# Optimization experiments

Hardware: AMD Instinct MI355X
Metric: run time of the kernel (lower is better)

Reference implementation:

```python
import jax, jax.numpy as jnp
import numpy as np

GROUP_SIZE = 128  # in_features // scales.shape[1]


def setup_inputs() -> dict:
    key = jax.random.key(0)
    kA, kq, ks, kz, kb = jax.random.split(key, 5)
    M, K, N = 2048, 4096, 4096
    G = K // GROUP_SIZE  # 32 groups
    A = jax.random.normal(kA, (M, K), dtype=jnp.float32)
    # unpacked uint4 quantized weights, values in [0, 16)
    qweight = jax.random.randint(kq, (N, K), 0, 16, dtype=jnp.int32)
    # per-group scales (typical GPTQ magnitude) and zero-points (float, 'original' zeros_mode)
    scales = jax.random.uniform(ks, (N, G), dtype=jnp.float32) * 0.02
    zeros = jax.random.uniform(kz, (N, G), dtype=jnp.float32) * 15.0
    bias = jax.random.normal(kb, (N,), dtype=jnp.float32)
    return {"A": A, "qweight": qweight, "scales": scales, "zeros": zeros, "bias": bias}


def reference(A, qweight, scales, zeros, bias):
    # Dequant: W[n,k] = (q[n,k] - zeros[n, k//gs]) * scales[n, k//gs]
    N, K = qweight.shape
    gs = K // scales.shape[1]
    s = jnp.repeat(scales, gs, axis=1)  # [N, K]
    z = jnp.repeat(zeros, gs, axis=1)   # [N, K]
    W = (qweight.astype(A.dtype) - z) * s
    # out[m,n] = sum_k A[m,k] * W[n,k] + bias[n]
    return jnp.einsum("mk,nk->mn", A, W) + bias
```

## Files before the change

kernel.cpp:

```cpp
#include <hip/hip_runtime.h>
#include <cstdint>
#include <cstddef>

#define MM 2048
#define KK 4096
#define NN 4096
#define GG 32
#define BM 128
#define BN 256
#define BK 64
#define NTILES (KK / BK)

typedef _Float16 half8_t __attribute__((ext_vector_type(8)));
typedef _Float16 half4_t __attribute__((ext_vector_type(4)));
typedef float f32x4 __attribute__((ext_vector_type(4)));

__device__ __forceinline__ void load_lds16(const void* gptr, void* lptr) {
  __builtin_amdgcn_global_load_lds(
      (const __attribute__((address_space(1))) unsigned int*)gptr,
      (__attribute__((address_space(3))) unsigned int*)lptr, 16, 0, 0);
}

#define ACNT8 (MM * KK / 8)
__global__ void prep_kernel(const float* __restrict__ A, const int* __restrict__ q,
                            const float* __restrict__ scales, const float* __restrict__ zeros,
                            _Float16* __restrict__ Ah, _Float16* __restrict__ Wh) {
  const int i = blockIdx.x * blockDim.x + threadIdx.x;
  if (i < ACNT8) {
    const float4 v0 = ((const float4*)A)[2 * (size_t)i];
    const float4 v1 = ((const float4*)A)[2 * (size_t)i + 1];
    half8_t h;
    h[0] = (_Float16)v0.x; h[1] = (_Float16)v0.y; h[2] = (_Float16)v0.z; h[3] = (_Float16)v0.w;
    h[4] = (_Float16)v1.x; h[5] = (_Float16)v1.y; h[6] = (_Float16)v1.z; h[7] = (_Float16)v1.w;
    *(half8_t*)(Ah + 8 * (size_t)i) = h;
  } else {
    const int j = i - ACNT8;
    const int e = j << 3;
    const int n = e >> 12;
    const int k = e & (KK - 1);
    const int g = k >> 7;
    const float sc = scales[(n << 5) + g];
    const float zp = zeros[(n << 5) + g];
    const float nzs = -zp * sc;
    const int4 q0 = ((const int4*)q)[2 * (size_t)j];
    const int4 q1 = ((const int4*)q)[2 * (size_t)j + 1];
    half8_t h;
    h[0] = (_Float16)fmaf((float)q0.x, sc, nzs);
    h[1] = (_Float16)fmaf((float)q0.y, sc, nzs);
    h[2] = (_Float16)fmaf((float)q0.z, sc, nzs);
    h[3] = (_Float16)fmaf((float)q0.w, sc, nzs);
    h[4] = (_Float16)fmaf((float)q1.x, sc, nzs);
    h[5] = (_Float16)fmaf((float)q1.y, sc, nzs);
    h[6] = (_Float16)fmaf((float)q1.z, sc, nzs);
    h[7] = (_Float16)fmaf((float)q1.w, sc, nzs);
    *(half8_t*)(Wh + (size_t)e) = h;
  }
}

__global__ __launch_bounds__(512, 2)
void gemm8_kernel(const _Float16* __restrict__ Ah, const _Float16* __restrict__ Wh,
                  const float* __restrict__ bias, float* __restrict__ out)
{
  __shared__ __align__(16) _Float16 sA[3][BM * BK];
  __shared__ __align__(16) _Float16 sB[3][BN * BK];

  const int tid = threadIdx.x;
  const int lane = tid & 63;
  const int wave = tid >> 6;
  const int wr = wave >> 2;
  const int wc = wave & 3;
  const int lr = lane & 15, quad = lane >> 4;

  const int bid = blockIdx.x;
  const int xcd = bid & 7;
  const int slot = bid >> 3;
  const int mt = slot >> 1;
  const int nt = xcd * 2 + (slot & 1);
  const int m0 = mt * BM;
  const int n0 = nt * BN;

  const int srow = lane >> 3, scc = lane & 7, gch = scc ^ srow;

  f32x4 acc[4][4];
#pragma unroll
  for (int i = 0; i < 4; ++i)
#pragma unroll
    for (int j = 0; j < 4; ++j) acc[i][j] = (f32x4){0.f, 0.f, 0.f, 0.f};

  auto stageA = [&](int t, int buf, int i) {
    load_lds16(Ah + (size_t)(m0 + i * 64 + (wave << 3) + srow) * KK + t * BK + (gch << 3),
               (void*)&sA[buf][(i * 64 + (wave << 3)) * BK]);
  };
  auto stageB = [&](int t, int buf, int i) {
    load_lds16(Wh + (size_t)(n0 + i * 64 + (wave << 3) + srow) * KK + t * BK + (gch << 3),
               (void*)&sB[buf][(i * 64 + (wave << 3)) * BK]);
  };

  stageB(0, 0, 0); stageB(0, 0, 1); stageA(0, 0, 0);
  stageB(0, 0, 2); stageB(0, 0, 3); stageA(0, 0, 1);
  stageB(1, 1, 0); stageB(1, 1, 1); stageA(1, 1, 0);
  stageB(1, 1, 2); stageB(1, 1, 3); stageA(1, 1, 1);
  asm volatile("s_waitcnt vmcnt(6)" ::: "memory");
  __builtin_amdgcn_s_barrier();

  int cur = 0, nb = 2;
  for (int t = 0; t < NTILES; ++t) {
    const _Float16* pA = sA[cur];
    const _Float16* pB = sB[cur];
    const bool st = (t < NTILES - 2);
    half8_t a0[2][2], a1[2][2], b[4][2];

#pragma unroll
    for (int x = 0; x < 2; ++x) {
      const _Float16* ba = &pA[(wr * 64 + x * 16 + lr) * BK];
#pragma unroll
      for (int ks = 0; ks < 2; ++ks)
        a0[x][ks] = *(const half8_t*)&ba[((ks * 4 + quad) ^ (lr & 7)) * 8];
    }
#pragma unroll
    for (int ni = 0; ni < 4; ++ni) {
      const _Float16* bb = &pB[(wc * 64 + ni * 16 + lr) * BK];
#pragma unroll
      for (int ks = 0; ks < 2; ++ks)
        b[ni][ks] = *(const half8_t*)&bb[((ks * 4 + quad) ^ (lr & 7)) * 8];
    }
    if (st) { stageB(t + 2, nb, 0); stageB(t + 2, nb, 1); stageA(t + 2, nb, 0); }
    __builtin_amdgcn_sched_barrier(0);
    __builtin_amdgcn_s_barrier();
    __builtin_amdgcn_s_setprio(1);
#pragma unroll
    for (int x = 0; x < 2; ++x)
#pragma unroll
      for (int ni = 0; ni < 4; ++ni) {
        acc[x][ni] = __builtin_amdgcn_mfma_f32_16x16x32_f16(a0[x][0], b[ni][0], acc[x][ni], 0, 0, 0);
        acc[x][ni] = __builtin_amdgcn_mfma_f32_16x16x32_f16(a0[x][1], b[ni][1], acc[x][ni], 0, 0, 0);
      }
    __builtin_amdgcn_s_setprio(0);
    __builtin_amdgcn_s_barrier();

#pragma unroll
    for (int x = 0; x < 2; ++x) {
      const _Float16* ba = &pA[(wr * 64 + (x + 2) * 16 + lr) * BK];
#pragma unroll
      for (int ks = 0; ks < 2; ++ks)
        a1[x][ks] = *(const half8_t*)&ba[((ks * 4 + quad) ^ (lr & 7)) * 8];
    }
    if (st) { stageB(t + 2, nb, 2); stageB(t + 2, nb, 3); stageA(t + 2, nb, 1); }
    __builtin_amdgcn_sched_barrier(0);
    __builtin_amdgcn_s_barrier();
    __builtin_amdgcn_s_setprio(1);
#pragma unroll
    for (int x = 0; x < 2; ++x)
#pragma unroll
      for (int ni = 0; ni < 4; ++ni) {
        acc[x + 2][ni] = __builtin_amdgcn_mfma_f32_16x16x32_f16(a1[x][0], b[ni][0], acc[x + 2][ni], 0, 0, 0);
        acc[x + 2][ni] = __builtin_amdgcn_mfma_f32_16x16x32_f16(a1[x][1], b[ni][1], acc[x + 2][ni], 0, 0, 0);
      }
    __builtin_amdgcn_s_setprio(0);
    if (t < NTILES - 2) asm volatile("s_waitcnt vmcnt(6)" ::: "memory");
    else                asm volatile("s_waitcnt vmcnt(0)" ::: "memory");
    __builtin_amdgcn_s_barrier();
    cur = (cur == 2) ? 0 : cur + 1;
    nb  = (nb  == 2) ? 0 : nb + 1;
  }

#pragma unroll
  for (int ni = 0; ni < 4; ++ni) {
    const int n = n0 + wc * 64 + ni * 16 + lr;
    const float bv = bias[n];
#pragma unroll
    for (int mi = 0; mi < 4; ++mi) {
      const int mbase = m0 + wr * 64 + mi * 16 + quad * 4;
#pragma unroll
      for (int r = 0; r < 4; ++r)
        out[(size_t)(mbase + r) * NN + n] = acc[mi][ni][r] + bv;
    }
  }
}

__global__ __launch_bounds__(256, 2)
void gemm_fused_kernel(const float* __restrict__ Af, const int* __restrict__ qw,
                       const float* __restrict__ scales, const float* __restrict__ zeros,
                       const float* __restrict__ bias, float* __restrict__ out)
{
  __shared__ __align__(16) _Float16 sA[128 * 64];
  __shared__ __align__(16) _Float16 sB[128 * 64];

  const int tid = threadIdx.x;
  const int lane = tid & 63;
  const int wave = tid >> 6;
  const int wr = wave >> 1, wc = wave & 1;

  const int bid = blockIdx.x;
  const int xcd = bid & 7;
  const int slot = bid >> 3;
  const int mt = slot >> 2;
  const int nt = xcd * 4 + (slot & 3);
  const int m0 = mt * 128;
  const int n0 = nt * 128;

  const int lr = lane & 15, quad = lane >> 4;

  f32x4 acc[4][4];
#pragma unroll
  for (int i = 0; i < 4; ++i)
#pragma unroll
    for (int j = 0; j < 4; ++j) acc[i][j] = (f32x4){0.f, 0.f, 0.f, 0.f};

  const int frow = tid >> 4;
  const int fc4 = tid & 15;

  for (int kt = 0; kt < KK / 64; ++kt) {
    const int k0 = kt * 64;
    const int g = k0 >> 7;
#pragma unroll
    for (int p = 0; p < 8; ++p) {
      const int row = p * 16 + frow;
      const int pc = (fc4 >> 1) ^ (row & 7);
      const int dst = row * 64 + pc * 8 + (fc4 & 1) * 4;
      const float4 avf = *(const float4*)&Af[(size_t)(m0 + row) * KK + k0 + fc4 * 4];
      half4_t ah;
      ah[0] = (_Float16)avf.x; ah[1] = (_Float16)avf.y;
      ah[2] = (_Float16)avf.z; ah[3] = (_Float16)avf.w;
      *(half4_t*)&sA[dst] = ah;
      const int n = n0 + row;
      const float sc = scales[(n << 5) + g];
      const float zp = zeros[(n << 5) + g];
      const float nzs = -zp * sc;
      const int4 qv = *(const int4*)&qw[(size_t)n * KK + k0 + fc4 * 4];
      half4_t bh;
      bh[0] = (_Float16)fmaf((float)qv.x, sc, nzs);
      bh[1] = (_Float16)fmaf((float)qv.y, sc, nzs);
      bh[2] = (_Float16)fmaf((float)qv.z, sc, nzs);
      bh[3] = (_Float16)fmaf((float)qv.w, sc, nzs);
      *(half4_t*)&sB[dst] = bh;
    }
    __syncthreads();
#pragma unroll
    for (int ks = 0; ks < 2; ++ks) {
      half8_t a[4], b[4];
#pragma unroll
      for (int t = 0; t < 4; ++t) {
        const int rA = wr * 64 + t * 16 + lr;
        const int j = ks * 4 + quad;
        a[t] = *(const half8_t*)&sA[rA * 64 + ((j ^ (lr & 7)) * 8)];
        const int rB = wc * 64 + t * 16 + lr;
        b[t] = *(const half8_t*)&sB[rB * 64 + ((j ^ (lr & 7)) * 8)];
      }
#pragma unroll
      for (int mi = 0; mi < 4; ++mi)
#pragma unroll
        for (int ni = 0; ni < 4; ++ni)
          acc[mi][ni] = __builtin_amdgcn_mfma_f32_16x16x32_f16(a[mi], b[ni], acc[mi][ni], 0, 0, 0);
    }
    __syncthreads();
  }

#pragma unroll
  for (int ni = 0; ni < 4; ++ni) {
    const int n = n0 + wc * 64 + ni * 16 + lr;
    const float bv = bias[n];
#pragma unroll
    for (int mi = 0; mi < 4; ++mi) {
      const int mbase = m0 + wr * 64 + mi * 16 + quad * 4;
#pragma unroll
      for (int r = 0; r < 4; ++r)
        out[(size_t)(mbase + r) * NN + n] = acc[mi][ni][r] + bv;
    }
  }
}

extern "C" void kernel_launch(void* const* d_in, const int* in_sizes, int n_in,
                              void* d_out, int out_size, void* d_ws, size_t ws_size,
                              hipStream_t stream) {
  (void)in_sizes; (void)n_in; (void)out_size;
  const float* A      = (const float*)d_in[0];
  const int*   qw     = (const int*)d_in[1];
  const float* scales = (const float*)d_in[2];
  const float* zeros  = (const float*)d_in[3];
  const float* bias   = (const float*)d_in[4];
  float* out = (float*)d_out;

  const size_t needA = (size_t)MM * KK * sizeof(_Float16);
  const size_t needW = (size_t)NN * KK * sizeof(_Float16);

  if (ws_size >= needA + needW) {
    _Float16* Ah = (_Float16*)d_ws;
    _Float16* Wh = (_Float16*)((char*)d_ws + needA);
    prep_kernel<<<((MM + NN) * KK / 8) / 256, 256, 0, stream>>>(A, qw, scales, zeros, Ah, Wh);
    gemm8_kernel<<<dim3(MM / BM * NN / BN), dim3(512), 0, stream>>>(Ah, Wh, bias, out);
  } else {
    gemm_fused_kernel<<<dim3(512), dim3(256), 0, stream>>>(A, qw, scales, zeros, bias, out);
  }
}
```

Before: 207.7 us.

## Store weights as uint8 and dequantize in-register inside the GEMM mainloop

The prep kernel now packs the int32 quantized weights to bytes and writes a transposed table of fp16 scale/offset pairs, instead of materializing a full fp16 weight matrix. The GEMM stages the byte weights and all scale/offset pairs into LDS, then dequantizes each fragment in registers using the 0x6400 magic-number fp16 trick before the MFMAs. This halves the weight traffic written by prep and read by the GEMM. In exchange it adds ALU work to the inner loop, rebalances the staging schedule and wait counts, and moves scale and offset math to fp16, which changes rounding.

```diff
diff --git a/kernel.cpp b/kernel.cpp
--- a/kernel.cpp
+++ b/kernel.cpp
@@ -13,6 +13,7 @@
 
 typedef _Float16 half8_t __attribute__((ext_vector_type(8)));
 typedef _Float16 half4_t __attribute__((ext_vector_type(4)));
+typedef _Float16 half2_t __attribute__((ext_vector_type(2)));
 typedef float f32x4 __attribute__((ext_vector_type(4)));
 
 __device__ __forceinline__ void load_lds16(const void* gptr, void* lptr) {
@@ -21,10 +22,35 @@
       (__attribute__((address_space(3))) unsigned int*)lptr, 16, 0, 0);
 }
 
+__device__ __forceinline__ half2_t h2_from_u32(unsigned v) {
+  union { unsigned u; half2_t h; } x; x.u = v; return x.h;
+}
+
+__device__ __forceinline__ half8_t dq8(unsigned d0, unsigned d1,
+                                       half2_t s2, half2_t c2) {
+  const unsigned M = 0x64006400u;
+  const half2_t off = (half2_t){(_Float16)1024.0f, (_Float16)1024.0f};
+  unsigned u0 = M | ((d0 & 0xFFu)         | ((d0 & 0xFF00u) << 8));
+  unsigned u1 = M | (((d0 >> 16) & 0xFFu) | ((d0 >> 24) << 16));
+  unsigned u2 = M | ((d1 & 0xFFu)         | ((d1 & 0xFF00u) << 8));
+  unsigned u3 = M | (((d1 >> 16) & 0xFFu) | ((d1 >> 24) << 16));
+  half2_t w0 = (h2_from_u32(u0) - off) * s2 + c2;
+  half2_t w1 = (h2_from_u32(u1) - off) * s2 + c2;
+  half2_t w2 = (h2_from_u32(u2) - off) * s2 + c2;
+  half2_t w3 = (h2_from_u32(u3) - off) * s2 + c2;
+  half8_t r;
+  r[0] = w0[0]; r[1] = w0[1]; r[2] = w1[0]; r[3] = w1[1];
+  r[4] = w2[0]; r[5] = w2[1]; r[6] = w3[0]; r[7] = w3[1];
+  return r;
+}
+
 #define ACNT8 (MM * KK / 8)
+#define WCNT8 (NN * KK / 8)
+#define SZCNT (NN * GG)
 __global__ void prep_kernel(const float* __restrict__ A, const int* __restrict__ q,
                             const float* __restrict__ scales, const float* __restrict__ zeros,
-                            _Float16* __restrict__ Ah, _Float16* __restrict__ Wh) {
+                            _Float16* __restrict__ Ah, unsigned char* __restrict__ Wq,
+                            unsigned* __restrict__ SZT) {
   const int i = blockIdx.x * blockDim.x + threadIdx.x;
   if (i < ACNT8) {
     const float4 v0 = ((const float4*)A)[2 * (size_t)i];
@@ -33,36 +59,35 @@
     h[0] = (_Float16)v0.x; h[1] = (_Float16)v0.y; h[2] = (_Float16)v0.z; h[3] = (_Float16)v0.w;
     h[4] = (_Float16)v1.x; h[5] = (_Float16)v1.y; h[6] = (_Float16)v1.z; h[7] = (_Float16)v1.w;
     *(half8_t*)(Ah + 8 * (size_t)i) = h;
-  } else {
+  } else if (i < ACNT8 + WCNT8) {
     const int j = i - ACNT8;
-    const int e = j << 3;
-    const int n = e >> 12;
-    const int k = e & (KK - 1);
-    const int g = k >> 7;
-    const float sc = scales[(n << 5) + g];
-    const float zp = zeros[(n << 5) + g];
-    const float nzs = -zp * sc;
     const int4 q0 = ((const int4*)q)[2 * (size_t)j];
     const int4 q1 = ((const int4*)q)[2 * (size_t)j + 1];
-    half8_t h;
-    h[0] = (_Float16)fmaf((float)q0.x, sc, nzs);
-    h[1] = (_Float16)fmaf((float)q0.y, sc, nzs);
-    h[2] = (_Float16)fmaf((float)q0.z, sc, nzs);
-    h[3] = (_Float16)fmaf((float)q0.w, sc, nzs);
-    h[4] = (_Float16)fmaf((float)q1.x, sc, nzs);
-    h[5] = (_Float16)fmaf((float)q1.y, sc, nzs);
-    h[6] = (_Float16)fmaf((float)q1.z, sc, nzs);
-    h[7] = (_Float16)fmaf((float)q1.w, sc, nzs);
-    *(half8_t*)(Wh + (size_t)e) = h;
+    uint2 p;
+    p.x = (q0.x & 0xFFu) | ((q0.y & 0xFFu) << 8) | ((q0.z & 0xFFu) << 16) | ((unsigned)(q0.w & 0xFFu) << 24);
+    p.y = (q1.x & 0xFFu) | ((q1.y & 0xFFu) << 8) | ((q1.z & 0xFFu) << 16) | ((unsigned)(q1.w & 0xFFu) << 24);
+    ((uint2*)Wq)[j] = p;
+  } else {
+    const int e = i - ACNT8 - WCNT8;
+    const int n = e >> 5;
+    const int g = e & 31;
+    const float s = scales[e];
+    const float z = zeros[e];
+    const float c = -z * s;
+    union { _Float16 h; unsigned short u; } sh, ch;
+    sh.h = (_Float16)s; ch.h = (_Float16)c;
+    SZT[(size_t)g * NN + n] = (unsigned)sh.u | ((unsigned)ch.u << 16);
   }
 }
 
 __global__ __launch_bounds__(512, 2)
-void gemm8_kernel(const _Float16* __restrict__ Ah, const _Float16* __restrict__ Wh,
+void gemm8_kernel(const _Float16* __restrict__ Ah, const unsigned char* __restrict__ Wq,
+                  const unsigned* __restrict__ SZT,
                   const float* __restrict__ bias, float* __restrict__ out)
 {
   __shared__ __align__(16) _Float16 sA[3][BM * BK];
-  __shared__ __align__(16) _Float16 sB[3][BN * BK];
+  __shared__ __align__(16) unsigned char sBq[3][BN * BK];
+  __shared__ __align__(16) unsigned sSZ[GG * BN];
 
   const int tid = threadIdx.x;
   const int lane = tid & 63;
@@ -79,7 +104,8 @@
   const int m0 = mt * BM;
   const int n0 = nt * BN;
 
-  const int srow = lane >> 3, scc = lane & 7, gch = scc ^ srow;
+  const int srow = lane >> 3, scc = lane & 7, gchA = scc ^ srow;
+  const int brow = lane >> 2, bcc = lane & 3;
 
   f32x4 acc[4][4];
 #pragma unroll
@@ -88,26 +114,40 @@
     for (int j = 0; j < 4; ++j) acc[i][j] = (f32x4){0.f, 0.f, 0.f, 0.f};
 
   auto stageA = [&](int t, int buf, int i) {
-    load_lds16(Ah + (size_t)(m0 + i * 64 + (wave << 3) + srow) * KK + t * BK + (gch << 3),
+    load_lds16(Ah + (size_t)(m0 + i * 64 + (wave << 3) + srow) * KK + t * BK + (gchA << 3),
                (void*)&sA[buf][(i * 64 + (wave << 3)) * BK]);
   };
-  auto stageB = [&](int t, int buf, int i) {
-    load_lds16(Wh + (size_t)(n0 + i * 64 + (wave << 3) + srow) * KK + t * BK + (gch << 3),
-               (void*)&sB[buf][(i * 64 + (wave << 3)) * BK]);
+  auto stageB = [&](int t, int buf, int c) {
+    const int r = c * 128 + (wave << 4) + brow;
+    const int g16 = bcc ^ ((r >> 1) & 3);
+    load_lds16(Wq + (size_t)(n0 + r) * KK + t * BK + g16 * 16,
+               (void*)&sBq[buf][(c * 128 + (wave << 4)) * BK]);
   };
-
-  stageB(0, 0, 0); stageB(0, 0, 1); stageA(0, 0, 0);
-  stageB(0, 0, 2); stageB(0, 0, 3); stageA(0, 0, 1);
-  stageB(1, 1, 0); stageB(1, 1, 1); stageA(1, 1, 0);
-  stageB(1, 1, 2); stageB(1, 1, 3); stageA(1, 1, 1);
-  asm volatile("s_waitcnt vmcnt(6)" ::: "memory");
+  auto stageSZ = [&](int c) {
+    const int g = c * 8 + wave;
+    load_lds16(SZT + (size_t)g * NN + n0 + lane * 4, (void*)&sSZ[g * BN]);
+  };
+
+  stageSZ(0); stageSZ(1); stageSZ(2); stageSZ(3);
+  stageB(0, 0, 0); stageB(0, 0, 1); stageA(0, 0, 0); stageA(0, 0, 1);
+  stageB(1, 1, 0); stageB(1, 1, 1); stageA(1, 1, 0); stageA(1, 1, 1);
+  asm volatile("s_waitcnt vmcnt(4)" ::: "memory");
   __builtin_amdgcn_s_barrier();
 
+  unsigned szv[4];
   int cur = 0, nb = 2;
   for (int t = 0; t < NTILES; ++t) {
     const _Float16* pA = sA[cur];
-    const _Float16* pB = sB[cur];
+    const unsigned char* pB = sBq[cur];
     const bool st = (t < NTILES - 2);
+
+    if ((t & 1) == 0) {
+      const int g = t >> 1;
+#pragma unroll
+      for (int ni = 0; ni < 4; ++ni)
+        szv[ni] = sSZ[g * BN + wc * 64 + ni * 16 + lr];
+    }
+
     half8_t a0[2][2], a1[2][2], b[4][2];
 
 #pragma unroll
@@ -119,12 +159,18 @@
     }
 #pragma unroll
     for (int ni = 0; ni < 4; ++ni) {
-      const _Float16* bb = &pB[(wc * 64 + ni * 16 + lr) * BK];
-#pragma unroll
-      for (int ks = 0; ks < 2; ++ks)
-        b[ni][ks] = *(const half8_t*)&bb[((ks * 4 + quad) ^ (lr & 7)) * 8];
-    }
-    if (st) { stageB(t + 2, nb, 0); stageB(t + 2, nb, 1); stageA(t + 2, nb, 0); }
+      const int row = wc * 64 + ni * 16 + lr;
+      const half2_t sc = h2_from_u32(szv[ni]);
+      const half2_t s2 = (half2_t){sc[0], sc[0]};
+      const half2_t c2 = (half2_t){sc[1], sc[1]};
+#pragma unroll
+      for (int ks = 0; ks < 2; ++ks) {
+        const int p8 = (ks * 4 + quad) ^ (row & 6);
+        const uint2 d = *(const uint2*)&pB[row * BK + p8 * 8];
+        b[ni][ks] = dq8(d.x, d.y, s2, c2);
+      }
+    }
+    if (st) { stageB(t + 2, nb, 0); stageB(t + 2, nb, 1); }
     __builtin_amdgcn_sched_barrier(0);
     __builtin_amdgcn_s_barrier();
     __builtin_amdgcn_s_setprio(1);
@@ -145,7 +191,7 @@
       for (int ks = 0; ks < 2; ++ks)
         a1[x][ks] = *(const half8_t*)&ba[((ks * 4 + quad) ^ (lr & 7)) * 8];
     }
-    if (st) { stageB(t + 2, nb, 2); stageB(t + 2, nb, 3); stageA(t + 2, nb, 1); }
+    if (st) { stageA(t + 2, nb, 0); stageA(t + 2, nb, 1); }
     __builtin_amdgcn_sched_barrier(0);
     __builtin_amdgcn_s_barrier();
     __builtin_amdgcn_s_setprio(1);
@@ -157,7 +203,7 @@
         acc[x + 2][ni] = __builtin_amdgcn_mfma_f32_16x16x32_f16(a1[x][1], b[ni][1], acc[x + 2][ni], 0, 0, 0);
       }
     __builtin_amdgcn_s_setprio(0);
-    if (t < NTILES - 2) asm volatile("s_waitcnt vmcnt(6)" ::: "memory");
+    if (t < NTILES - 2) asm volatile("s_waitcnt vmcnt(4)" ::: "memory");
     else                asm volatile("s_waitcnt vmcnt(0)" ::: "memory");
     __builtin_amdgcn_s_barrier();
     cur = (cur == 2) ? 0 : cur + 1;
@@ -281,14 +327,16 @@
   const float* bias   = (const float*)d_in[4];
   float* out = (float*)d_out;
 
-  const size_t needA = (size_t)MM * KK * sizeof(_Float16);
-  const size_t needW = (size_t)NN * KK * sizeof(_Float16);
-
-  if (ws_size >= needA + needW) {
-    _Float16* Ah = (_Float16*)d_ws;
-    _Float16* Wh = (_Float16*)((char*)d_ws + needA);
-    prep_kernel<<<((MM + NN) * KK / 8) / 256, 256, 0, stream>>>(A, qw, scales, zeros, Ah, Wh);
-    gemm8_kernel<<<dim3(MM / BM * NN / BN), dim3(512), 0, stream>>>(Ah, Wh, bias, out);
+  const size_t needA  = (size_t)MM * KK * sizeof(_Float16);
+  const size_t needWq = (size_t)NN * KK;
+  const size_t needSZ = (size_t)NN * GG * sizeof(unsigned);
+
+  if (ws_size >= needA + needWq + needSZ) {
+    _Float16*      Ah  = (_Float16*)d_ws;
+    unsigned char* Wq  = (unsigned char*)d_ws + needA;
+    unsigned*      SZT = (unsigned*)((char*)d_ws + needA + needWq);
+    prep_kernel<<<(ACNT8 + WCNT8 + SZCNT) / 256, 256, 0, stream>>>(A, qw, scales, zeros, Ah, Wq, SZT);
+    gemm8_kernel<<<dim3(MM / BM * NN / BN), dim3(512), 0, stream>>>(Ah, Wq, SZT, bias, out);
   } else {
     gemm_fused_kernel<<<dim3(512), dim3(256), 0, stream>>>(A, qw, scales, zeros, bias, out);
   }
```

Result: slower. 239.1 us (+15.1%).

## Use 4-wave blocks with 64x128 warp tiles and BK=32 single-phase loop

Applied to the files above, without the earlier changes.

Rewrites the fp16 GEMM main kernel to use 256 threads (4 waves), each computing a 64x128 output tile with 32 accumulators, and halves the K tile to 32. Each iteration now issues one MFMA phase with a single barrier instead of two split phases with several barriers. The swizzled LDS layout is dropped in favour of plain row addressing. The aim is more MFMA work per LDS fragment load and fewer barriers per tile. The costs are higher register pressure, twice as many K iterations, and possible LDS bank conflicts from the unswizzled reads.

```diff
diff --git a/kernel.cpp b/kernel.cpp
--- a/kernel.cpp
+++ b/kernel.cpp
@@ -8,7 +8,7 @@
 #define GG 32
 #define BM 128
 #define BN 256
-#define BK 64
+#define BK 32
 #define NTILES (KK / BK)
 
 typedef _Float16 half8_t __attribute__((ext_vector_type(8)));
@@ -57,9 +57,9 @@
   }
 }
 
-__global__ __launch_bounds__(512, 2)
-void gemm8_kernel(const _Float16* __restrict__ Ah, const _Float16* __restrict__ Wh,
-                  const float* __restrict__ bias, float* __restrict__ out)
+__global__ __launch_bounds__(256, 2)
+void gemm12_kernel(const _Float16* __restrict__ Ah, const _Float16* __restrict__ Wh,
+                   const float* __restrict__ bias, float* __restrict__ out)
 {
   __shared__ __align__(16) _Float16 sA[3][BM * BK];
   __shared__ __align__(16) _Float16 sB[3][BN * BK];
@@ -67,8 +67,8 @@
   const int tid = threadIdx.x;
   const int lane = tid & 63;
   const int wave = tid >> 6;
-  const int wr = wave >> 2;
-  const int wc = wave & 3;
+  const int wr = wave >> 1;
+  const int wc = wave & 1;
   const int lr = lane & 15, quad = lane >> 4;
 
   const int bid = blockIdx.x;
@@ -79,27 +79,29 @@
   const int m0 = mt * BM;
   const int n0 = nt * BN;
 
-  const int srow = lane >> 3, scc = lane & 7, gch = scc ^ srow;
-
-  f32x4 acc[4][4];
+  const int srow = lane >> 2, sch = lane & 3;
+
+  f32x4 acc[4][8];
 #pragma unroll
   for (int i = 0; i < 4; ++i)
 #pragma unroll
-    for (int j = 0; j < 4; ++j) acc[i][j] = (f32x4){0.f, 0.f, 0.f, 0.f};
+    for (int j = 0; j < 8; ++j) acc[i][j] = (f32x4){0.f, 0.f, 0.f, 0.f};
 
   auto stageA = [&](int t, int buf, int i) {
-    load_lds16(Ah + (size_t)(m0 + i * 64 + (wave << 3) + srow) * KK + t * BK + (gch << 3),
-               (void*)&sA[buf][(i * 64 + (wave << 3)) * BK]);
+    const int r16 = (wave * 2 + i) * 16;
+    load_lds16(Ah + (size_t)(m0 + r16 + srow) * KK + t * BK + sch * 8,
+               (void*)&sA[buf][r16 * BK]);
   };
-  auto stageB = [&](int t, int buf, int i) {
-    load_lds16(Wh + (size_t)(n0 + i * 64 + (wave << 3) + srow) * KK + t * BK + (gch << 3),
-               (void*)&sB[buf][(i * 64 + (wave << 3)) * BK]);
+  auto stageB = [&](int t, int buf, int c) {
+    const int r16 = (wave * 4 + c) * 16;
+    load_lds16(Wh + (size_t)(n0 + r16 + srow) * KK + t * BK + sch * 8,
+               (void*)&sB[buf][r16 * BK]);
   };
 
-  stageB(0, 0, 0); stageB(0, 0, 1); stageA(0, 0, 0);
-  stageB(0, 0, 2); stageB(0, 0, 3); stageA(0, 0, 1);
-  stageB(1, 1, 0); stageB(1, 1, 1); stageA(1, 1, 0);
-  stageB(1, 1, 2); stageB(1, 1, 3); stageA(1, 1, 1);
+  stageB(0, 0, 0); stageB(0, 0, 1); stageB(0, 0, 2); stageB(0, 0, 3);
+  stageA(0, 0, 0); stageA(0, 0, 1);
+  stageB(1, 1, 0); stageB(1, 1, 1); stageB(1, 1, 2); stageB(1, 1, 3);
+  stageA(1, 1, 0); stageA(1, 1, 1);
   asm volatile("s_waitcnt vmcnt(6)" ::: "memory");
   __builtin_amdgcn_s_barrier();
 
@@ -108,55 +110,29 @@
     const _Float16* pA = sA[cur];
     const _Float16* pB = sB[cur];
     const bool st = (t < NTILES - 2);
-    half8_t a0[2][2], a1[2][2], b[4][2];
-
-#pragma unroll
-    for (int x = 0; x < 2; ++x) {
-      const _Float16* ba = &pA[(wr * 64 + x * 16 + lr) * BK];
-#pragma unroll
-      for (int ks = 0; ks < 2; ++ks)
-        a0[x][ks] = *(const half8_t*)&ba[((ks * 4 + quad) ^ (lr & 7)) * 8];
-    }
-#pragma unroll
-    for (int ni = 0; ni < 4; ++ni) {
-      const _Float16* bb = &pB[(wc * 64 + ni * 16 + lr) * BK];
-#pragma unroll
-      for (int ks = 0; ks < 2; ++ks)
-        b[ni][ks] = *(const half8_t*)&bb[((ks * 4 + quad) ^ (lr & 7)) * 8];
-    }
-    if (st) { stageB(t + 2, nb, 0); stageB(t + 2, nb, 1); stageA(t + 2, nb, 0); }
+
+    half8_t a[4], b[8];
+#pragma unroll
+    for (int mi = 0; mi < 4; ++mi)
+      a[mi] = *(const half8_t*)&pA[(wr * 64 + mi * 16 + lr) * BK + quad * 8];
+#pragma unroll
+    for (int ni = 0; ni < 8; ++ni)
+      b[ni] = *(const half8_t*)&pB[(wc * 128 + ni * 16 + lr) * BK + quad * 8];
+
+    if (st) {
+      stageB(t + 2, nb, 0); stageB(t + 2, nb, 1); stageB(t + 2, nb, 2); stageB(t + 2, nb, 3);
+      stageA(t + 2, nb, 0); stageA(t + 2, nb, 1);
+    }
     __builtin_amdgcn_sched_barrier(0);
-    __builtin_amdgcn_s_barrier();
+
     __builtin_amdgcn_s_setprio(1);
 #pragma unroll
-    for (int x = 0; x < 2; ++x)
-#pragma unroll
-      for (int ni = 0; ni < 4; ++ni) {
-        acc[x][ni] = __builtin_amdgcn_mfma_f32_16x16x32_f16(a0[x][0], b[ni][0], acc[x][ni], 0, 0, 0);
-        acc[x][ni] = __builtin_amdgcn_mfma_f32_16x16x32_f16(a0[x][1], b[ni][1], acc[x][ni], 0, 0, 0);
-      }
+    for (int mi = 0; mi < 4; ++mi)
+#pragma unroll
+      for (int ni = 0; ni < 8; ++ni)
+        acc[mi][ni] = __builtin_amdgcn_mfma_f32_16x16x32_f16(a[mi], b[ni], acc[mi][ni], 0, 0, 0);
     __builtin_amdgcn_s_setprio(0);
-    __builtin_amdgcn_s_barrier();
-
-#pragma unroll
-    for (int x = 0; x < 2; ++x) {
-      const _Float16* ba = &pA[(wr * 64 + (x + 2) * 16 + lr) * BK];
-#pragma unroll
-      for (int ks = 0; ks < 2; ++ks)
-        a1[x][ks] = *(const half8_t*)&ba[((ks * 4 + quad) ^ (lr & 7)) * 8];
-    }
-    if (st) { stageB(t + 2, nb, 2); stageB(t + 2, nb, 3); stageA(t + 2, nb, 1); }
-    __builtin_amdgcn_sched_barrier(0);
-    __builtin_amdgcn_s_barrier();
-    __builtin_amdgcn_s_setprio(1);
-#pragma unroll
-    for (int x = 0; x < 2; ++x)
-#pragma unroll
-      for (int ni = 0; ni < 4; ++ni) {
-        acc[x + 2][ni] = __builtin_amdgcn_mfma_f32_16x16x32_f16(a1[x][0], b[ni][0], acc[x + 2][ni], 0, 0, 0);
-        acc[x + 2][ni] = __builtin_amdgcn_mfma_f32_16x16x32_f16(a1[x][1], b[ni][1], acc[x + 2][ni], 0, 0, 0);
-      }
-    __builtin_amdgcn_s_setprio(0);
+
     if (t < NTILES - 2) asm volatile("s_waitcnt vmcnt(6)" ::: "memory");
     else                asm volatile("s_waitcnt vmcnt(0)" ::: "memory");
     __builtin_amdgcn_s_barrier();
@@ -165,8 +141,8 @@
   }
 
 #pragma unroll
-  for (int ni = 0; ni < 4; ++ni) {
-    const int n = n0 + wc * 64 + ni * 16 + lr;
+  for (int ni = 0; ni < 8; ++ni) {
+    const int n = n0 + wc * 128 + ni * 16 + lr;
     const float bv = bias[n];
 #pragma unroll
     for (int mi = 0; mi < 4; ++mi) {
@@ -288,7 +264,7 @@
     _Float16* Ah = (_Float16*)d_ws;
     _Float16* Wh = (_Float16*)((char*)d_ws + needA);
     prep_kernel<<<((MM + NN) * KK / 8) / 256, 256, 0, stream>>>(A, qw, scales, zeros, Ah, Wh);
-    gemm8_kernel<<<dim3(MM / BM * NN / BN), dim3(512), 0, stream>>>(Ah, Wh, bias, out);
+    gemm12_kernel<<<dim3(MM / BM * NN / BN), dim3(256), 0, stream>>>(Ah, Wh, bias, out);
   } else {
     gemm_fused_kernel<<<dim3(512), dim3(256), 0, stream>>>(A, qw, scales, zeros, bias, out);
   }
```

New measurement: 231.0 us. +11.2%, slower.

## Use 256x256 tiles with split-K of two plus a reduction kernel

Applied to the files above, without the earlier changes.

Adds a new GEMM kernel with 256x256 output tiles per block. The K dimension is split into two halves so the launch still has 256 blocks. Each half writes its partial sums to either the output or a workspace buffer, and a separate reduce kernel adds the two together with the bias. The larger tile raises arithmetic intensity and cuts global/LDS traffic per FLOP. The cost is an extra 32 MB fp32 partial written and read back, an extra launch, and heavier register use (128 accumulator floats per lane) with one block per CU. It runs only when the workspace is large enough; otherwise the old gemm8 path is used.

```diff
diff --git a/kernel.cpp b/kernel.cpp
--- a/kernel.cpp
+++ b/kernel.cpp
@@ -6,10 +6,6 @@
 #define KK 4096
 #define NN 4096
 #define GG 32
-#define BM 128
-#define BN 256
-#define BK 64
-#define NTILES (KK / BK)
 
 typedef _Float16 half8_t __attribute__((ext_vector_type(8)));
 typedef _Float16 half4_t __attribute__((ext_vector_type(4)));
@@ -57,12 +53,13 @@
   }
 }
 
-__global__ __launch_bounds__(512, 2)
-void gemm8_kernel(const _Float16* __restrict__ Ah, const _Float16* __restrict__ Wh,
-                  const float* __restrict__ bias, float* __restrict__ out)
+#define KTILES 32
+__global__ __launch_bounds__(512)
+void gemm16_kernel(const _Float16* __restrict__ Ah, const _Float16* __restrict__ Wh,
+                   float* __restrict__ out, float* __restrict__ P1)
 {
-  __shared__ __align__(16) _Float16 sA[3][BM * BK];
-  __shared__ __align__(16) _Float16 sB[3][BN * BK];
+  __shared__ __align__(16) _Float16 sA[2][256 * 64];
+  __shared__ __align__(16) _Float16 sB[2][256 * 64];
 
   const int tid = threadIdx.x;
   const int lane = tid & 63;
@@ -74,10 +71,149 @@
   const int bid = blockIdx.x;
   const int xcd = bid & 7;
   const int slot = bid >> 3;
+  const int kh = slot >> 4;
+  const int nt = slot & 15;
+  const int m0 = xcd * 256;
+  const int n0 = nt * 256;
+  const int khBase = kh * (KK / 2);
+
+  const int srow = lane >> 3, scc = lane & 7, gch = scc ^ srow;
+
+  f32x4 acc[8][4];
+#pragma unroll
+  for (int i = 0; i < 8; ++i)
+#pragma unroll
+    for (int j = 0; j < 4; ++j) acc[i][j] = (f32x4){0.f, 0.f, 0.f, 0.f};
+
+  auto stA = [&](int t, int buf, int c) {
+    load_lds16(Ah + (size_t)(m0 + c * 64 + (wave << 3) + srow) * KK + khBase + t * 64 + (gch << 3),
+               (void*)&sA[buf][(c * 64 + (wave << 3)) * 64]);
+  };
+  auto stB = [&](int t, int buf, int c) {
+    load_lds16(Wh + (size_t)(n0 + c * 64 + (wave << 3) + srow) * KK + khBase + t * 64 + (gch << 3),
+               (void*)&sB[buf][(c * 64 + (wave << 3)) * 64]);
+  };
+#define EARLY6(T, BUF) do { stA((T), (BUF), 0); stA((T), (BUF), 2); \
+    stB((T), (BUF), 0); stB((T), (BUF), 1); stB((T), (BUF), 2); stB((T), (BUF), 3); } while (0)
+#define LATE2(T, BUF)  do { stA((T), (BUF), 1); stA((T), (BUF), 3); } while (0)
+
+  EARLY6(0, 0); LATE2(0, 0);
+  asm volatile("s_waitcnt vmcnt(2)" ::: "memory");
+  __builtin_amdgcn_s_barrier();
+
+  for (int t = 0; t < KTILES; ++t) {
+    const int bufc = t & 1, bufn = bufc ^ 1;
+    const _Float16* pA = sA[bufc];
+    const _Float16* pB = sB[bufc];
+    const bool more = (t + 1 < KTILES);
+
+    half8_t a[4][2], b[4][2];
+#pragma unroll
+    for (int mf = 0; mf < 4; ++mf) {
+      const _Float16* ba = &pA[(wr * 128 + mf * 16 + lr) * 64];
+#pragma unroll
+      for (int ks = 0; ks < 2; ++ks)
+        a[mf][ks] = *(const half8_t*)&ba[((ks * 4 + quad) ^ (lr & 7)) * 8];
+    }
+#pragma unroll
+    for (int nf = 0; nf < 4; ++nf) {
+      const _Float16* bb = &pB[(wc * 64 + nf * 16 + lr) * 64];
+#pragma unroll
+      for (int ks = 0; ks < 2; ++ks)
+        b[nf][ks] = *(const half8_t*)&bb[((ks * 4 + quad) ^ (lr & 7)) * 8];
+    }
+    if (more) EARLY6(t + 1, bufn);
+    __builtin_amdgcn_sched_barrier(0);
+    __builtin_amdgcn_s_setprio(1);
+#pragma unroll
+    for (int mf = 0; mf < 4; ++mf)
+#pragma unroll
+      for (int nf = 0; nf < 4; ++nf) {
+        acc[mf][nf] = __builtin_amdgcn_mfma_f32_16x16x32_f16(a[mf][0], b[nf][0], acc[mf][nf], 0, 0, 0);
+        acc[mf][nf] = __builtin_amdgcn_mfma_f32_16x16x32_f16(a[mf][1], b[nf][1], acc[mf][nf], 0, 0, 0);
+      }
+    __builtin_amdgcn_s_setprio(0);
+
+    if (more) asm volatile("s_waitcnt vmcnt(6)" ::: "memory");
+    else      asm volatile("s_waitcnt vmcnt(0)" ::: "memory");
+    __builtin_amdgcn_s_barrier();
+
+    half8_t ah[4][2];
+#pragma unroll
+    for (int mf = 0; mf < 4; ++mf) {
+      const _Float16* ba = &pA[(wr * 128 + (mf + 4) * 16 + lr) * 64];
+#pragma unroll
+      for (int ks = 0; ks < 2; ++ks)
+        ah[mf][ks] = *(const half8_t*)&ba[((ks * 4 + quad) ^ (lr & 7)) * 8];
+    }
+    if (more) LATE2(t + 1, bufn);
+    __builtin_amdgcn_sched_barrier(0);
+    __builtin_amdgcn_s_setprio(1);
+#pragma unroll
+    for (int mf = 0; mf < 4; ++mf)
+#pragma unroll
+      for (int nf = 0; nf < 4; ++nf) {
+        acc[mf + 4][nf] = __builtin_amdgcn_mfma_f32_16x16x32_f16(ah[mf][0], b[nf][0], acc[mf + 4][nf], 0, 0, 0);
+        acc[mf + 4][nf] = __builtin_amdgcn_mfma_f32_16x16x32_f16(ah[mf][1], b[nf][1], acc[mf + 4][nf], 0, 0, 0);
+      }
+    __builtin_amdgcn_s_setprio(0);
+
+    if (more) asm volatile("s_waitcnt vmcnt(2)" ::: "memory");
+    else      asm volatile("s_waitcnt vmcnt(0)" ::: "memory");
+    __builtin_amdgcn_s_barrier();
+  }
+
+#undef EARLY6
+#undef LATE2
+
+  float* dst = (kh == 0) ? out : P1;
+#pragma unroll
+  for (int nf = 0; nf < 4; ++nf) {
+    const int n = n0 + wc * 64 + nf * 16 + lr;
+#pragma unroll
+    for (int mf = 0; mf < 8; ++mf) {
+      const int mbase = m0 + wr * 128 + mf * 16 + quad * 4;
+#pragma unroll
+      for (int r = 0; r < 4; ++r)
+        dst[(size_t)(mbase + r) * NN + n] = acc[mf][nf][r];
+    }
+  }
+}
+
+__global__ void reduce_kernel(float* __restrict__ out, const float* __restrict__ P1,
+                              const float* __restrict__ bias) {
+  const int i = blockIdx.x * blockDim.x + threadIdx.x;
+  const int n = (i * 4) & (NN - 1);
+  const float4 o = ((const float4*)out)[i];
+  const float4 p = ((const float4*)P1)[i];
+  const float4 b = *(const float4*)&bias[n];
+  float4 r;
+  r.x = o.x + p.x + b.x; r.y = o.y + p.y + b.y;
+  r.z = o.z + p.z + b.z; r.w = o.w + p.w + b.w;
+  ((float4*)out)[i] = r;
+}
+
+__global__ __launch_bounds__(512, 2)
+void gemm8_kernel(const _Float16* __restrict__ Ah, const _Float16* __restrict__ Wh,
+                  const float* __restrict__ bias, float* __restrict__ out)
+{
+  __shared__ __align__(16) _Float16 sA[3][128 * 64];
+  __shared__ __align__(16) _Float16 sB[3][256 * 64];
+
+  const int tid = threadIdx.x;
+  const int lane = tid & 63;
+  const int wave = tid >> 6;
+  const int wr = wave >> 2;
+  const int wc = wave & 3;
+  const int lr = lane & 15, quad = lane >> 4;
+
+  const int bid = blockIdx.x;
+  const int xcd = bid & 7;
+  const int slot = bid >> 3;
   const int mt = slot >> 1;
   const int nt = xcd * 2 + (slot & 1);
-  const int m0 = mt * BM;
-  const int n0 = nt * BN;
+  const int m0 = mt * 128;
+  const int n0 = nt * 256;
 
   const int srow = lane >> 3, scc = lane & 7, gch = scc ^ srow;
 
@@ -88,12 +224,12 @@
     for (int j = 0; j < 4; ++j) acc[i][j] = (f32x4){0.f, 0.f, 0.f, 0.f};
 
   auto stageA = [&](int t, int buf, int i) {
-    load_lds16(Ah + (size_t)(m0 + i * 64 + (wave << 3) + srow) * KK + t * BK + (gch << 3),
-               (void*)&sA[buf][(i * 64 + (wave << 3)) * BK]);
+    load_lds16(Ah + (size_t)(m0 + i * 64 + (wave << 3) + srow) * KK + t * 64 + (gch << 3),
+               (void*)&sA[buf][(i * 64 + (wave << 3)) * 64]);
   };
   auto stageB = [&](int t, int buf, int i) {
-    load_lds16(Wh + (size_t)(n0 + i * 64 + (wave << 3) + srow) * KK + t * BK + (gch << 3),
-               (void*)&sB[buf][(i * 64 + (wave << 3)) * BK]);
+    load_lds16(Wh + (size_t)(n0 + i * 64 + (wave << 3) + srow) * KK + t * 64 + (gch << 3),
+               (void*)&sB[buf][(i * 64 + (wave << 3)) * 64]);
   };
 
   stageB(0, 0, 0); stageB(0, 0, 1); stageA(0, 0, 0);
@@ -104,22 +240,22 @@
   __builtin_amdgcn_s_barrier();
 
   int cur = 0, nb = 2;
-  for (int t = 0; t < NTILES; ++t) {
+  for (int t = 0; t < 64; ++t) {
     const _Float16* pA = sA[cur];
     const _Float16* pB = sB[cur];
-    const bool st = (t < NTILES - 2);
+    const bool st = (t < 62);
     half8_t a0[2][2], a1[2][2], b[4][2];
 
 #pragma unroll
     for (int x = 0; x < 2; ++x) {
-      const _Float16* ba = &pA[(wr * 64 + x * 16 + lr) * BK];
+      const _Float16* ba = &pA[(wr * 64 + x * 16 + lr) * 64];
 #pragma unroll
       for (int ks = 0; ks < 2; ++ks)
         a0[x][ks] = *(const half8_t*)&ba[((ks * 4 + quad) ^ (lr & 7)) * 8];
     }
 #pragma unroll
     for (int ni = 0; ni < 4; ++ni) {
-      const _Float16* bb = &pB[(wc * 64 + ni * 16 + lr) * BK];
+      const _Float16* bb = &pB[(wc * 64 + ni * 16 + lr) * 64];
 #pragma unroll
       for (int ks = 0; ks < 2; ++ks)
         b[ni][ks] = *(const half8_t*)&bb[((ks * 4 + quad) ^ (lr & 7)) * 8];
@@ -140,7 +276,7 @@
 
 #pragma unroll
     for (int x = 0; x < 2; ++x) {
-      const _Float16* ba = &pA[(wr * 64 + (x + 2) * 16 + lr) * BK];
+      const _Float16* ba = &pA[(wr * 64 + (x + 2) * 16 + lr) * 64];
 #pragma unroll
       for (int ks = 0; ks < 2; ++ks)
         a1[x][ks] = *(const half8_t*)&ba[((ks * 4 + quad) ^ (lr & 7)) * 8];
@@ -157,8 +293,8 @@
         acc[x + 2][ni] = __builtin_amdgcn_mfma_f32_16x16x32_f16(a1[x][1], b[ni][1], acc[x + 2][ni], 0, 0, 0);
       }
     __builtin_amdgcn_s_setprio(0);
-    if (t < NTILES - 2) asm volatile("s_waitcnt vmcnt(6)" ::: "memory");
-    else                asm volatile("s_waitcnt vmcnt(0)" ::: "memory");
+    if (t < 62) asm volatile("s_waitcnt vmcnt(6)" ::: "memory");
+    else        asm volatile("s_waitcnt vmcnt(0)" ::: "memory");
     __builtin_amdgcn_s_barrier();
     cur = (cur == 2) ? 0 : cur + 1;
     nb  = (nb  == 2) ? 0 : nb + 1;
@@ -283,12 +419,20 @@
 
   const size_t needA = (size_t)MM * KK * sizeof(_Float16);
   const size_t needW = (size_t)NN * KK * sizeof(_Float16);
-
-  if (ws_size >= needA + needW) {
+  const size_t needP = (size_t)MM * NN * sizeof(float);
+
+  if (ws_size >= needA + needW + needP) {
+    _Float16* Ah = (_Float16*)d_ws;
+    _Float16* Wh = (_Float16*)((char*)d_ws + needA);
+    float*    P1 = (float*)((char*)d_ws + needA + needW);
+    prep_kernel<<<((MM + NN) * KK / 8) / 256, 256, 0, stream>>>(A, qw, scales, zeros, Ah, Wh);
+    gemm16_kernel<<<dim3(256), dim3(512), 0, stream>>>(Ah, Wh, out, P1);
+    reduce_kernel<<<dim3(MM * NN / 4 / 256), dim3(256), 0, stream>>>(out, P1, bias);
+  } else if (ws_size >= needA + needW) {
     _Float16* Ah = (_Float16*)d_ws;
     _Float16* Wh = (_Float16*)((char*)d_ws + needA);
     prep_kernel<<<((MM + NN) * KK / 8) / 256, 256, 0, stream>>>(A, qw, scales, zeros, Ah, Wh);
-    gemm8_kernel<<<dim3(MM / BM * NN / BN), dim3(512), 0, stream>>>(Ah, Wh, bias, out);
+    gemm8_kernel<<<dim3(256), dim3(512), 0, stream>>>(Ah, Wh, bias, out);
   } else {
     gemm_fused_kernel<<<dim3(512), dim3(256), 0, stream>>>(A, qw, scales, zeros, bias, out);
   }
```

After: 220.2 us. +6.0%, slower.
